# Performance work log

Hardware: AMD Instinct MI355X
Metric: run time of the kernel (lower is better)

## Reference

```python
import jax, jax.numpy as jnp
import numpy as np

N_CONCEPTS = 32
D_MODEL = 512
COMMITMENT_COST = 0.25


def setup_inputs() -> dict:
    key = jax.random.key(0)
    kx, kc = jax.random.split(key)
    x = jax.random.normal(kx, (8, 8192, D_MODEL), dtype=jnp.float32)
    codebook = jax.random.normal(kc, (N_CONCEPTS, D_MODEL), dtype=jnp.float32) * 0.02
    return {"x": x, "codebook": codebook}


def reference(x, codebook):
    B, T, D = x.shape
    x_flat = x.reshape(B * T, D)
    x2 = jnp.sum(x_flat * x_flat, axis=1, keepdims=True)          # [BT,1]
    c2 = jnp.sum(codebook * codebook, axis=1)                      # [K]
    xc = jnp.einsum('nd,kd->nk', x_flat, codebook)                 # [BT,K]
    dists = x2 + c2 - 2.0 * xc
    nearest_idx = jnp.argmin(dists, axis=1)                        # [BT]
    q = codebook[nearest_idx]                                      # gather [BT,D]
    # straight-through estimator
    quantized = x_flat + jax.lax.stop_gradient(q - x_flat)
    vq_loss = (jnp.mean((jax.lax.stop_gradient(quantized) - x_flat) ** 2)
               + COMMITMENT_COST * jnp.mean((quantized - jax.lax.stop_gradient(x_flat)) ** 2))
    # histogram of concept usage (fused replacement of the per-concept loop)
    counts = jnp.zeros((N_CONCEPTS,), dtype=jnp.int32).at[nearest_idx].add(1)
    return quantized.reshape(B, T, D), vq_loss, counts
```

## Files before the change

### kernel.cpp

```cpp
#include <hip/hip_runtime.h>

#define BT_ROWS 65536
#define DIM     512
#define NK      32
#define TPB     128
#define RPB     64
#define NBLK    (BT_ROWS / RPB)
#define CHUNK   32
#define NCHUNK  (DIM / CHUNK)

typedef float f4 __attribute__((ext_vector_type(4)));
typedef float f32x16 __attribute__((ext_vector_type(16)));
typedef short bf16x8 __attribute__((ext_vector_type(8)));
typedef unsigned int u32x4 __attribute__((ext_vector_type(4)));

union Frag { u32x4 q; unsigned int w[4]; bf16x8 v; };


__global__ void vq_prep(const float* __restrict__ cb, float* __restrict__ c2,
                        int* __restrict__ counts, unsigned int* __restrict__ cbh32) {
    int t = threadIdx.x;
    const f4* c4 = (const f4*)cb;
#pragma unroll
    for (int i = 0; i < 16; ++i) {
        f4 v = c4[t * 16 + i];
        unsigned int w0, w1;
        asm("v_cvt_pk_bf16_f32 %0, %1, %2" : "=v"(w0) : "v"(v.x), "v"(v.y));
        asm("v_cvt_pk_bf16_f32 %0, %1, %2" : "=v"(w1) : "v"(v.z), "v"(v.w));
        cbh32[t * 32 + 2 * i]     = w0;
        cbh32[t * 32 + 2 * i + 1] = w1;
    }
    if (t < NK) {
        float s = 0.f;
#pragma unroll 8
        for (int i = 0; i < DIM / 4; ++i) {
            f4 v = c4[t * (DIM / 4) + i];
            s += v.x * v.x + v.y * v.y + v.z * v.z + v.w * v.w;
        }
        c2[t] = s;
    } else if (t < 2 * NK) {
        counts[t - NK] = 0;
    }
}

__global__ __launch_bounds__(TPB, 2) void vq_main(const float* __restrict__ x,
                                                  const float* __restrict__ cb,
                                                  const float* __restrict__ c2,
                                                  const unsigned short* __restrict__ cbh,
                                                  float* __restrict__ out,
                                                  float* __restrict__ blockloss,
                                                  int* __restrict__ counts) {
    const int tid  = threadIdx.x;
    const int lane = tid & 63;
    const int wv   = tid >> 6;
    const int tb   = wv * 32;
    const int R0   = blockIdx.x * RPB;

    __shared__ float         xbuf[2][RPB][CHUNK];
    __shared__ float         bestd[RPB];
    __shared__ float         x2row[RPB];
    __shared__ unsigned char karr[RPB];
    __shared__ int           hist[NK];
    if (tid < NK) hist[tid] = 0;

    const char* xsrc[4];
    int         ldsoff[4];
#pragma unroll
    for (int t = 0; t < 4; ++t) {
        int rl    = tb + t * 8 + (lane >> 3);
        xsrc[t]   = (const char*)x + (size_t)(R0 + rl) * (DIM * 4) + (lane & 7) * 16;
        ldsoff[t] = rl * CHUNK + (((lane & 7) ^ (lane >> 3)) << 2);
    }
    float* const lds0 = &xbuf[0][0][0];

    f4 rs[3][4];
#define GLOAD(c) do {                                                            \
    _Pragma("unroll")                                                            \
    for (int t = 0; t < 4; ++t)                                                  \
        rs[(c) % 3][t] = *(const f4*)(xsrc[t] + (size_t)(c) * 128);              \
} while (0)
#define DSWRITE(c) do {                                                          \
    _Pragma("unroll")                                                            \
    for (int t = 0; t < 4; ++t)                                                  \
        *(f4*)(lds0 + (((c) & 1) * (RPB * CHUNK)) + ldsoff[t]) = rs[(c) % 3][t]; \
} while (0)

    f32x16 acc;
#pragma unroll
    for (int r = 0; r < 16; ++r) acc[r] = 0.f;
    float x2acc = 0.f;

    const int m   = tb + (lane & 31);
    const int sw  = m & 7;
    const int n   = lane & 31;
    const int kh  = (lane >> 5) << 3;
    const float c2v = c2[n];

    GLOAD(0); GLOAD(1); GLOAD(2);
    DSWRITE(0);

#pragma unroll
    for (int c = 0; c < NCHUNK; ++c) {
        if (c + 3 < NCHUNK) GLOAD(c + 3);
        if (c + 1 < NCHUNK) DSWRITE(c + 1);

        const f4* xrow = (const f4*)&xbuf[c & 1][m][0];
#pragma unroll
        for (int s = 0; s < 2; ++s) {
            const int tg = s * 4 + ((lane >> 5) << 1);
            f4 a0 = xrow[tg ^ sw];
            f4 a1 = xrow[(tg + 1) ^ sw];
            x2acc += a0.x * a0.x + a0.y * a0.y + a0.z * a0.z + a0.w * a0.w
                   + a1.x * a1.x + a1.y * a1.y + a1.z * a1.z + a1.w * a1.w;

            Frag fa;
            asm("v_cvt_pk_bf16_f32 %0, %1, %2" : "=v"(fa.w[0]) : "v"(a0.x), "v"(a0.y));
            asm("v_cvt_pk_bf16_f32 %0, %1, %2" : "=v"(fa.w[1]) : "v"(a0.z), "v"(a0.w));
            asm("v_cvt_pk_bf16_f32 %0, %1, %2" : "=v"(fa.w[2]) : "v"(a1.x), "v"(a1.y));
            asm("v_cvt_pk_bf16_f32 %0, %1, %2" : "=v"(fa.w[3]) : "v"(a1.z), "v"(a1.w));

            Frag fb;
            fb.q = *(const u32x4*)(cbh + (size_t)n * DIM + c * CHUNK + s * 16 + kh);

            acc = __builtin_amdgcn_mfma_f32_32x32x16_bf16(fa.v, fb.v, acc, 0, 0, 0);
        }
    }
#undef GLOAD
#undef DSWRITE

    {
        float o = __shfl_xor(x2acc, 32, 64);
        if (lane < 32) x2row[tb + lane] = x2acc + o;
    }

#pragma unroll
    for (int r = 0; r < 16; ++r) {
        float val = c2v - 2.f * acc[r];
        int   idx = n;
#pragma unroll
        for (int off = 1; off <= 16; off <<= 1) {
            float ov = __shfl_xor(val, off, 64);
            int   oi = __shfl_xor(idx, off, 64);
            if (ov < val || (ov == val && oi < idx)) { val = ov; idx = oi; }
        }
        const int mrow = tb + (r & 3) + 8 * (r >> 2) + ((lane >> 5) << 2);
        if ((lane & 31) == 0) { bestd[mrow] = val; karr[mrow] = (unsigned char)idx; }
    }
    __syncthreads();

    if (tid < RPB) {
        float ls = x2row[tid] + bestd[tid];
        atomicAdd(&hist[karr[tid]], 1);
#pragma unroll
        for (int mo = 32; mo; mo >>= 1) ls += __shfl_xor(ls, mo, 64);
        if (tid == 0) blockloss[blockIdx.x] = ls;
    }
    __syncthreads();
    if (tid < NK) {
        int h = hist[tid];
        if (h) atomicAdd(&counts[tid], h);
    }

    const f4* __restrict__ cb4 = (const f4*)cb;
    f4* __restrict__ o4 = (f4*)out;
#pragma unroll 1
    for (int rr = 0; rr < 32; ++rr) {
        int    kr   = karr[tb + rr];
        size_t base = (size_t)(R0 + tb + rr) * (DIM / 4);
        o4[base + lane]      = cb4[kr * (DIM / 4) + lane];
        o4[base + 64 + lane] = cb4[kr * (DIM / 4) + 64 + lane];
    }
}

__global__ void vq_final(const float* __restrict__ blockloss, const int* __restrict__ counts,
                         float* __restrict__ out) {
    int   t = threadIdx.x;
    float v = blockloss[t] + blockloss[t + 256] + blockloss[t + 512] + blockloss[t + 768];
#pragma unroll
    for (int m = 32; m; m >>= 1) v += __shfl_xor(v, m, 64);
    __shared__ float red[4];
    if ((t & 63) == 0) red[t >> 6] = v;
    __syncthreads();
    if (t == 0)
        out[(size_t)BT_ROWS * DIM] =
            1.25f * (red[0] + red[1] + red[2] + red[3]) / (float)((size_t)BT_ROWS * DIM);
    if (t < NK)
        out[(size_t)BT_ROWS * DIM + 1 + t] = (float)counts[t];
}

extern "C" void kernel_launch(void* const* d_in, const int* in_sizes, int n_in,
                              void* d_out, int out_size, void* d_ws, size_t ws_size,
                              hipStream_t stream) {
    const float* x  = (const float*)d_in[0];
    const float* cb = (const float*)d_in[1];
    float* out = (float*)d_out;

    float* f         = (float*)d_ws;
    float* c2        = f;
    float* blockloss = f + NK;
    int*   counts    = (int*)(f + NK + NBLK);
    unsigned int*   cbh32 = (unsigned int*)((char*)d_ws + 8192);
    unsigned short* cbh   = (unsigned short*)cbh32;

    vq_prep<<<1, 256, 0, stream>>>(cb, c2, counts, cbh32);
    vq_main<<<NBLK, TPB, 0, stream>>>(x, cb, c2, cbh, out, blockloss, counts);
    vq_final<<<1, 256, 0, stream>>>(blockloss, counts, out);
}
```

Measured before the change: 72.50 us.

## Load x fragments directly into registers, one wave per block, drop LDS staging

Each block becomes a single 64-thread wave handling 32 rows. That wave loads its MFMA A fragments straight from global memory into a triple-buffered register queue, together with the prefetched codebook B fragments, so the LDS buffering and swizzling are gone. The argmin result, loss and histogram are now done inside the wave with shuffles, and each lane accumulates its own count before one atomic, which removes the shared-memory arrays and __syncthreads. The cost is twice as many blocks and less coalesced direct loads of 32-byte segments per lane, along with higher register pressure from keeping all 16 argmin results live.

```diff
diff --git a/kernel.cpp b/kernel.cpp
--- a/kernel.cpp
+++ b/kernel.cpp
@@ -3,11 +3,12 @@
 #define BT_ROWS 65536
 #define DIM     512
 #define NK      32
-#define TPB     128
-#define RPB     64
+#define TPB     64
+#define RPB     32
 #define NBLK    (BT_ROWS / RPB)
 #define CHUNK   32
 #define NCHUNK  (DIM / CHUNK)
+#define DQ      3
 
 typedef float f4 __attribute__((ext_vector_type(4)));
 typedef float f32x16 __attribute__((ext_vector_type(16)));
@@ -50,39 +51,23 @@
                                                   float* __restrict__ out,
                                                   float* __restrict__ blockloss,
                                                   int* __restrict__ counts) {
-    const int tid  = threadIdx.x;
-    const int lane = tid & 63;
-    const int wv   = tid >> 6;
-    const int tb   = wv * 32;
+    const int lane = threadIdx.x & 63;
+    const int n    = lane & 31;
+    const int hi   = lane >> 5;
     const int R0   = blockIdx.x * RPB;
 
-    __shared__ float         xbuf[2][RPB][CHUNK];
-    __shared__ float         bestd[RPB];
-    __shared__ float         x2row[RPB];
-    __shared__ unsigned char karr[RPB];
-    __shared__ int           hist[NK];
-    if (tid < NK) hist[tid] = 0;
+    const char* xb = (const char*)x + (size_t)(R0 + n) * (DIM * 4) + hi * 32;
+    const unsigned short* cbn = cbh + (size_t)n * DIM + hi * 8;
 
-    const char* xsrc[4];
-    int         ldsoff[4];
-#pragma unroll
-    for (int t = 0; t < 4; ++t) {
-        int rl    = tb + t * 8 + (lane >> 3);
-        xsrc[t]   = (const char*)x + (size_t)(R0 + rl) * (DIM * 4) + (lane & 7) * 16;
-        ldsoff[t] = rl * CHUNK + (((lane & 7) ^ (lane >> 3)) << 2);
-    }
-    float* const lds0 = &xbuf[0][0][0];
-
-    f4 rs[3][4];
-#define GLOAD(c) do {                                                            \
-    _Pragma("unroll")                                                            \
-    for (int t = 0; t < 4; ++t)                                                  \
-        rs[(c) % 3][t] = *(const f4*)(xsrc[t] + (size_t)(c) * 128);              \
-} while (0)
-#define DSWRITE(c) do {                                                          \
-    _Pragma("unroll")                                                            \
-    for (int t = 0; t < 4; ++t)                                                  \
-        *(f4*)(lds0 + (((c) & 1) * (RPB * CHUNK)) + ldsoff[t]) = rs[(c) % 3][t]; \
+    f4   rs[DQ][4];
+    Frag fr[DQ][2];
+#define GLOAD(c) do {                                                    \
+    rs[(c) % DQ][0] = *(const f4*)(xb + (c) * 128);                      \
+    rs[(c) % DQ][1] = *(const f4*)(xb + (c) * 128 + 16);                 \
+    rs[(c) % DQ][2] = *(const f4*)(xb + (c) * 128 + 64);                 \
+    rs[(c) % DQ][3] = *(const f4*)(xb + (c) * 128 + 80);                 \
+    fr[(c) % DQ][0].q = *(const u32x4*)(cbn + (c) * CHUNK);              \
+    fr[(c) % DQ][1].q = *(const u32x4*)(cbn + (c) * CHUNK + 16);         \
 } while (0)
 
     f32x16 acc;
@@ -90,92 +75,84 @@
     for (int r = 0; r < 16; ++r) acc[r] = 0.f;
     float x2acc = 0.f;
 
-    const int m   = tb + (lane & 31);
-    const int sw  = m & 7;
-    const int n   = lane & 31;
-    const int kh  = (lane >> 5) << 3;
-    const float c2v = c2[n];
-
     GLOAD(0); GLOAD(1); GLOAD(2);
-    DSWRITE(0);
 
 #pragma unroll
     for (int c = 0; c < NCHUNK; ++c) {
-        if (c + 3 < NCHUNK) GLOAD(c + 3);
-        if (c + 1 < NCHUNK) DSWRITE(c + 1);
+        f4   a0 = rs[c % DQ][0], a1 = rs[c % DQ][1];
+        f4   a2 = rs[c % DQ][2], a3 = rs[c % DQ][3];
+        Frag f0 = fr[c % DQ][0], f1 = fr[c % DQ][1];
+        if (c + DQ < NCHUNK) GLOAD(c + DQ);
 
-        const f4* xrow = (const f4*)&xbuf[c & 1][m][0];
+        x2acc += a0.x * a0.x + a0.y * a0.y + a0.z * a0.z + a0.w * a0.w
+               + a1.x * a1.x + a1.y * a1.y + a1.z * a1.z + a1.w * a1.w
+               + a2.x * a2.x + a2.y * a2.y + a2.z * a2.z + a2.w * a2.w
+               + a3.x * a3.x + a3.y * a3.y + a3.z * a3.z + a3.w * a3.w;
+
+        Frag fa;
+        asm("v_cvt_pk_bf16_f32 %0, %1, %2" : "=v"(fa.w[0]) : "v"(a0.x), "v"(a0.y));
+        asm("v_cvt_pk_bf16_f32 %0, %1, %2" : "=v"(fa.w[1]) : "v"(a0.z), "v"(a0.w));
+        asm("v_cvt_pk_bf16_f32 %0, %1, %2" : "=v"(fa.w[2]) : "v"(a1.x), "v"(a1.y));
+        asm("v_cvt_pk_bf16_f32 %0, %1, %2" : "=v"(fa.w[3]) : "v"(a1.z), "v"(a1.w));
+        acc = __builtin_amdgcn_mfma_f32_32x32x16_bf16(fa.v, f0.v, acc, 0, 0, 0);
+
+        Frag fb;
+        asm("v_cvt_pk_bf16_f32 %0, %1, %2" : "=v"(fb.w[0]) : "v"(a2.x), "v"(a2.y));
+        asm("v_cvt_pk_bf16_f32 %0, %1, %2" : "=v"(fb.w[1]) : "v"(a2.z), "v"(a2.w));
+        asm("v_cvt_pk_bf16_f32 %0, %1, %2" : "=v"(fb.w[2]) : "v"(a3.x), "v"(a3.y));
+        asm("v_cvt_pk_bf16_f32 %0, %1, %2" : "=v"(fb.w[3]) : "v"(a3.z), "v"(a3.w));
+        acc = __builtin_amdgcn_mfma_f32_32x32x16_bf16(fb.v, f1.v, acc, 0, 0, 0);
+    }
+#undef GLOAD
+
+    float x2tot = x2acc;
 #pragma unroll
-        for (int s = 0; s < 2; ++s) {
-            const int tg = s * 4 + ((lane >> 5) << 1);
-            f4 a0 = xrow[tg ^ sw];
-            f4 a1 = xrow[(tg + 1) ^ sw];
-            x2acc += a0.x * a0.x + a0.y * a0.y + a0.z * a0.z + a0.w * a0.w
-                   + a1.x * a1.x + a1.y * a1.y + a1.z * a1.z + a1.w * a1.w;
+    for (int mo = 1; mo <= 32; mo <<= 1) x2tot += __shfl_xor(x2tot, mo, 64);
 
-            Frag fa;
-            asm("v_cvt_pk_bf16_f32 %0, %1, %2" : "=v"(fa.w[0]) : "v"(a0.x), "v"(a0.y));
-            asm("v_cvt_pk_bf16_f32 %0, %1, %2" : "=v"(fa.w[1]) : "v"(a0.z), "v"(a0.w));
-            asm("v_cvt_pk_bf16_f32 %0, %1, %2" : "=v"(fa.w[2]) : "v"(a1.x), "v"(a1.y));
-            asm("v_cvt_pk_bf16_f32 %0, %1, %2" : "=v"(fa.w[3]) : "v"(a1.z), "v"(a1.w));
-
-            Frag fb;
-            fb.q = *(const u32x4*)(cbh + (size_t)n * DIM + c * CHUNK + s * 16 + kh);
-
-            acc = __builtin_amdgcn_mfma_f32_32x32x16_bf16(fa.v, fb.v, acc, 0, 0, 0);
+    const float c2v = c2[n];
+    float val[16]; int idx[16];
+#pragma unroll
+    for (int r = 0; r < 16; ++r) {
+        val[r] = c2v - 2.f * acc[r];
+        idx[r] = n;
+#pragma unroll
+        for (int off = 1; off <= 16; off <<= 1) {
+            float ov = __shfl_xor(val[r], off, 64);
+            int   oi = __shfl_xor(idx[r], off, 64);
+            if (ov < val[r] || (ov == val[r] && oi < idx[r])) { val[r] = ov; idx[r] = oi; }
         }
     }
-#undef GLOAD
-#undef DSWRITE
 
-    {
-        float o = __shfl_xor(x2acc, 32, 64);
-        if (lane < 32) x2row[tb + lane] = x2acc + o;
-    }
-
+    float lsum = 0.f;
 #pragma unroll
-    for (int r = 0; r < 16; ++r) {
-        float val = c2v - 2.f * acc[r];
-        int   idx = n;
-#pragma unroll
-        for (int off = 1; off <= 16; off <<= 1) {
-            float ov = __shfl_xor(val, off, 64);
-            int   oi = __shfl_xor(idx, off, 64);
-            if (ov < val || (ov == val && oi < idx)) { val = ov; idx = oi; }
-        }
-        const int mrow = tb + (r & 3) + 8 * (r >> 2) + ((lane >> 5) << 2);
-        if ((lane & 31) == 0) { bestd[mrow] = val; karr[mrow] = (unsigned char)idx; }
-    }
-    __syncthreads();
-
-    if (tid < RPB) {
-        float ls = x2row[tid] + bestd[tid];
-        atomicAdd(&hist[karr[tid]], 1);
-#pragma unroll
-        for (int mo = 32; mo; mo >>= 1) ls += __shfl_xor(ls, mo, 64);
-        if (tid == 0) blockloss[blockIdx.x] = ls;
-    }
-    __syncthreads();
-    if (tid < NK) {
-        int h = hist[tid];
-        if (h) atomicAdd(&counts[tid], h);
-    }
+    for (int r = 0; r < 16; ++r) lsum += val[r];
+    float lother = __shfl(lsum, 32, 64);
+    if (lane == 0) blockloss[blockIdx.x] = x2tot + lsum + lother;
 
     const f4* __restrict__ cb4 = (const f4*)cb;
     f4* __restrict__ o4 = (f4*)out;
-#pragma unroll 1
+    int cnt = 0;
+#pragma unroll
     for (int rr = 0; rr < 32; ++rr) {
-        int    kr   = karr[tb + rr];
-        size_t base = (size_t)(R0 + tb + rr) * (DIM / 4);
+        const int r = (rr & 3) | (((rr >> 3) & 3) << 2);
+        const int h = (rr >> 2) & 1;
+        int kr = __shfl(idx[r], h << 5, 64);
+        cnt += (kr == n) ? 1 : 0;
+        size_t base = (size_t)(R0 + rr) * (DIM / 4);
         o4[base + lane]      = cb4[kr * (DIM / 4) + lane];
         o4[base + 64 + lane] = cb4[kr * (DIM / 4) + 64 + lane];
     }
+    if (hi == 0 && cnt) atomicAdd(&counts[n], cnt);
+
+__asm__ volatile("" ::: "memory");
 }
 
 __global__ void vq_final(const float* __restrict__ blockloss, const int* __restrict__ counts,
                          float* __restrict__ out) {
     int   t = threadIdx.x;
-    float v = blockloss[t] + blockloss[t + 256] + blockloss[t + 512] + blockloss[t + 768];
+    float v = 0.f;
+#pragma unroll
+    for (int i = 0; i < NBLK / 256; ++i) v += blockloss[t + i * 256];
 #pragma unroll
     for (int m = 32; m; m >>= 1) v += __shfl_xor(v, m, 64);
     __shared__ float red[4];
@@ -199,7 +176,7 @@
     float* c2        = f;
     float* blockloss = f + NK;
     int*   counts    = (int*)(f + NK + NBLK);
-    unsigned int*   cbh32 = (unsigned int*)((char*)d_ws + 8192);
+    unsigned int*   cbh32 = (unsigned int*)((char*)d_ws + 16384);
     unsigned short* cbh   = (unsigned short*)cbh32;
 
     vq_prep<<<1, 256, 0, stream>>>(cb, c2, counts, cbh32);
```

Result: no change. 72.31 us (-0.3%).
